# Performance work log

Hardware: AMD Instinct MI355X
Metric: run time of the kernel (lower is better)

Reference implementation:

```python
import jax, jax.numpy as jnp
import numpy as np

_J6 = jnp.array([[0,0,0,0,0,1],[0,0,0,0,-1,0],[0,0,0,1,0,0],
                 [0,0,1,0,0,0],[0,-1,0,0,0,0],[1,0,0,0,0,0]], dtype=jnp.float32)
_PAIRS4 = [(0,1),(0,2),(0,3),(1,2),(1,3),(2,3)]  # combinations(range(4),2)


def exterior(p1, p2):
    # Plucker line coords of two 4-vectors, normalized. (...,4)x(...,4)->(...,6)
    parts = [p1[..., i] * p2[..., j] - p1[..., j] * p2[..., i] for i, j in _PAIRS4]
    L = jnp.stack(parts, axis=-1)
    n = jnp.maximum(jnp.linalg.norm(L, axis=-1, keepdims=True), 1e-12)
    return L / n


def setup_inputs() -> dict:
    key = jax.random.key(0)
    B, T, D, H = 2, 2048, 1024, 16
    ks = jax.random.split(key, 10)
    w = lambda k, shape: jax.random.normal(k, shape, jnp.float32) * 0.02
    return {
        "x": jax.random.normal(ks[0], (B, T, D), jnp.float32),
        "qkv_w": w(ks[1], (3 * D, D)),
        "qkv_b": jnp.zeros((3 * D,), jnp.float32),
        "w1w": w(ks[2], (4 * H, D)),
        "w2w": w(ks[3], (4 * H, D)),
        "r1w": w(ks[4], (4 * H, D)),
        "r2w": w(ks[5], (4 * H, D)),
        "memv_w": w(ks[6], (D, D)),
        "memv_b": jnp.zeros((D,), jnp.float32),
        "memg_w": w(ks[7], (H, D)),
        "memg_b": jnp.zeros((H,), jnp.float32),
        "mem_scale": jnp.full((H,), 0.1, jnp.float32),
        "iter_mix": jnp.array(0.0, jnp.float32),
        "out_w": w(ks[8], (D, D)),
        "out_b": jnp.zeros((D,), jnp.float32),
        "decay_logits": jnp.full((H,), 4.6, jnp.float32),
    }


def reference(x, qkv_w, qkv_b, w1w, w2w, r1w, r2w, memv_w, memv_b,
              memg_w, memg_b, mem_scale, iter_mix, out_w, out_b, decay_logits):
    B, T, D = x.shape
    H = decay_logits.shape[0]
    dh = D // H
    pd = 6
    scale = dh ** -0.5

    # --- standard causal softmax attention ---
    qkv = (x @ qkv_w.T + qkv_b).reshape(B, T, 3, H, dh)
    qkv = jnp.transpose(qkv, (2, 0, 3, 1, 4))  # (3,B,H,T,dh)
    q, k, v = qkv[0], qkv[1], qkv[2]
    scores = jnp.einsum('bhtd,bhsd->bhts', q, k) * scale
    causal = jnp.triu(jnp.ones((T, T), dtype=bool), 1)
    scores = jnp.where(causal, -jnp.inf, scores)
    attn = jax.nn.softmax(scores, axis=-1)  # dropout is identity in eval
    seq_out = jnp.einsum('bhts,bhsd->bhtd', attn, v)
    seq_out = jnp.transpose(seq_out, (0, 2, 1, 3)).reshape(B, T, D)

    # --- decay-weighted Gram memory (linear-attention style state) ---
    x_prev = jnp.concatenate([jnp.zeros((B, 1, D), x.dtype), x[:, :-1]], axis=1)
    w1 = (x_prev @ w1w.T).reshape(B, T, H, 4)
    w2 = (x @ w2w.T).reshape(B, T, H, 4)
    write_lines = exterior(w1, w2)  # (B,T,H,6)
    r1 = (x @ r1w.T).reshape(B, T, H, 4)
    r2 = (x @ r2w.T).reshape(B, T, H, 4)
    read_lines = exterior(r1, r2)

    Jw = jnp.einsum('bthi,ij->bhtj', write_lines, _J6)  # (B,H,T,6)
    rd = jnp.transpose(read_lines, (0, 2, 1, 3))        # (B,H,T,6)

    decays = jax.nn.sigmoid(decay_logits)               # (H,)
    pos = jnp.arange(T, dtype=x.dtype)
    outer = Jw[..., :, None] * Jw[..., None, :]         # (B,H,T,6,6)
    decay_inv = (1.0 / jnp.maximum(decays, 1e-6))[:, None] ** pos[None, :]  # (H,T)
    outer_scaled = outer * decay_inv[None, :, :, None, None]
    M_cumsum = jnp.cumsum(outer_scaled, axis=2)
    M_cumsum = jnp.concatenate(
        [jnp.zeros((B, H, 1, pd, pd), x.dtype), M_cumsum[:, :, :-1]], axis=2)
    decay_fwd = decays[:, None] ** pos[None, :]
    M_all = M_cumsum * decay_fwd[None, :, :, None, None]

    rd_M = jnp.einsum('bhti,bhtij->bhtj', rd, M_all)
    score_M = jnp.sum(rd_M * rd, axis=-1)    # (B,H,T)
    score_M2 = jnp.sum(rd_M * rd_M, axis=-1)
    alpha = jax.nn.sigmoid(iter_mix)
    mem_score = (1 - alpha) * score_M + alpha * score_M2

    mem_val = x @ memv_w.T + memv_b                     # (B,T,D)
    gate = jax.nn.sigmoid(x @ memg_w.T + memg_b)        # (B,T,H)
    mem_score_t = jnp.transpose(mem_score, (0, 2, 1))   # (B,T,H)
    gated = jax.nn.sigmoid(mem_score_t * mem_scale) * gate
    gated = jnp.mean(gated, axis=-1, keepdims=True)     # (B,T,1)

    return (seq_out + gated * mem_val) @ out_w.T + out_b
```

## Files before the change

kernel.cpp:

```cpp
#include <hip/hip_runtime.h>
#include <stdint.h>

#define TT 2048
#define DD 1024
#define HH 16
#define LDP 4368
#define SCH 64
#define SNC (TT/SCH)

using bf16x8 = __attribute__((ext_vector_type(8))) __bf16;
using u16x8  = __attribute__((ext_vector_type(8))) unsigned short;
using f32x4  = __attribute__((ext_vector_type(4))) float;

__device__ __forceinline__ float bf2f(unsigned short u){
  unsigned int x = ((unsigned int)u) << 16;
  return __builtin_bit_cast(float, x);
}
__device__ __forceinline__ unsigned short f2bf(float f){
  unsigned int x = __builtin_bit_cast(unsigned int, f);
  x += 0x7fffu + ((x >> 16) & 1u);
  return (unsigned short)(x >> 16);
}
__device__ __forceinline__ float sigmoidf_(float x){ return 1.0f/(1.0f+__expf(-x)); }

__device__ __forceinline__ void gload_lds16(const void* g, void* l){
  auto gp = (const __attribute__((address_space(1))) unsigned int*)(uintptr_t)g;
  auto lp = (__attribute__((address_space(3))) unsigned int*)(unsigned int)(uintptr_t)l;
  __builtin_amdgcn_global_load_lds(gp, lp, 16, 0, 0);
}

__global__ void prep_all_kernel(const float* __restrict__ qkv_w, const float* __restrict__ w1w,
                                const float* __restrict__ w2w, const float* __restrict__ r1w,
                                const float* __restrict__ r2w, const float* __restrict__ memv_w,
                                const float* __restrict__ memg_w, const float* __restrict__ out_w,
                                const float* __restrict__ qkv_b, const float* __restrict__ memv_b,
                                const float* __restrict__ memg_b, const float* __restrict__ x,
                                unsigned short* __restrict__ Wcat, float* __restrict__ bcat,
                                unsigned short* __restrict__ xb)
{
  const int blk = blockIdx.x;
  if (blk < 5392) {
    const int idx = blk*256 + threadIdx.x;
    {
      const int row = idx >> 8, c4 = (idx & 255)*4;
      const float* src; int r;
      if      (row < 3072) { src = qkv_w;  r = row; }
      else if (row < 3136) { src = w1w;    r = row-3072; }
      else if (row < 3200) { src = w2w;    r = row-3136; }
      else if (row < 3264) { src = r1w;    r = row-3200; }
      else if (row < 3328) { src = r2w;    r = row-3264; }
      else if (row < 4352) { src = memv_w; r = row-3328; }
      else if (row < 4368) { src = memg_w; r = row-4352; }
      else                 { src = out_w;  r = row-4368; }
      const float4 v = *(const float4*)(src + (size_t)r*1024 + c4);
      ushort4 o; o.x=f2bf(v.x); o.y=f2bf(v.y); o.z=f2bf(v.z); o.w=f2bf(v.w);
      *(ushort4*)(Wcat + (size_t)row*1024 + c4) = o;
    }
    if (idx < 4368) {
      float v;
      if      (idx < 3072) v = qkv_b[idx];
      else if (idx < 3328) v = 0.f;
      else if (idx < 4352) v = memv_b[idx-3328];
      else                 v = memg_b[idx-4352];
      bcat[idx] = v;
    }
  } else {
    const int idx = (blk - 5392)*256 + threadIdx.x;
    const float4 v = ((const float4*)x)[idx];
    ushort4 o; o.x=f2bf(v.x); o.y=f2bf(v.y); o.z=f2bf(v.z); o.w=f2bf(v.w);
    ((ushort4*)xb)[idx] = o;
  }
}

template<bool OUTF32>
__global__ __launch_bounds__(256, 3)
void gemm_bt_kernel(const unsigned short* __restrict__ A, int lda,
                    const unsigned short* __restrict__ Bt, int ldb,
                    const float* __restrict__ bias,
                    void* __restrict__ Cout, int ldc, int N, int K)
{
  __shared__ unsigned short smem[24576];
  const int tid = threadIdx.x;
  const int w = tid >> 6, lane = tid & 63;
  const int l15 = lane & 15, l4 = lane >> 4;
  const int m0 = blockIdx.x * 128;
  const int n0 = blockIdx.y * 128;
  const int wr = (w >> 1) * 64, wc = (w & 1) * 64;

  const f32x4 zero = {0.f,0.f,0.f,0.f};
  f32x4 acc[4][4];
#pragma unroll
  for (int i = 0; i < 4; ++i)
#pragma unroll
    for (int j = 0; j < 4; ++j) acc[i][j] = zero;

  const int srow = lane >> 2;
  const int k8   = (lane & 3) * 8;

  auto stage = [&](int k0, int buf) {
#pragma unroll
    for (int q = 0; q < 4; ++q) {
      const int c = q*4 + w;
      const int rloc = (c & 7)*16 + srow;
      if (c < 8) {
        gload_lds16(A + (size_t)(m0 + rloc)*lda + k0 + k8,
                    (char*)smem + buf*8192 + (c&7)*1024);
      } else {
        int nrow = n0 + rloc; if (nrow >= N) nrow = N - 1;
        gload_lds16(Bt + (size_t)nrow*ldb + k0 + k8,
                    (char*)smem + 24576 + buf*8192 + (c&7)*1024);
      }
    }
  };

  stage(0, 0);
  if (K > 32) stage(32, 1);

  int ti = 0;
  for (int k0 = 0; k0 < K; k0 += 32, ++ti) {
    if (k0 + 32 < K) { asm volatile("s_waitcnt vmcnt(4)" ::: "memory"); }
    else             { asm volatile("s_waitcnt vmcnt(0)" ::: "memory"); }
    __builtin_amdgcn_s_barrier();
    if (k0 + 64 < K) stage(k0 + 64, (ti + 2) % 3);

    const int cur = ti % 3;
    bf16x8 af[4], bfr[4];
#pragma unroll
    for (int i = 0; i < 4; ++i) {
      af[i]  = *reinterpret_cast<const bf16x8*>((const char*)smem + cur*8192
                 + (wr + i*16 + l15)*64 + l4*16);
      bfr[i] = *reinterpret_cast<const bf16x8*>((const char*)smem + 24576 + cur*8192
                 + (wc + i*16 + l15)*64 + l4*16);
    }
#pragma unroll
    for (int i = 0; i < 4; ++i)
#pragma unroll
      for (int j = 0; j < 4; ++j)
        acc[i][j] = __builtin_amdgcn_mfma_f32_16x16x32_bf16(af[i], bfr[j], acc[i][j], 0, 0, 0);
  }

  if (OUTF32) {
#pragma unroll
    for (int i = 0; i < 4; ++i) {
      const int rowb = m0 + wr + i*16 + l4*4;
#pragma unroll
      for (int j = 0; j < 4; ++j) {
        const int col = n0 + wc + j*16 + l15;
        if (col < N) {
          const float bv = bias ? bias[col] : 0.0f;
#pragma unroll
          for (int r = 0; r < 4; ++r)
            ((float*)Cout)[(size_t)(rowb + r)*ldc + col] = acc[i][j][r] + bv;
        }
      }
    }
  } else {
    __syncthreads();
#pragma unroll
    for (int i = 0; i < 4; ++i) {
      const int rloc = wr + i*16 + l4*4;
#pragma unroll
      for (int j = 0; j < 4; ++j) {
        const int col = wc + j*16 + l15;
        const float bv = bias ? bias[n0 + col] : 0.0f;
#pragma unroll
        for (int r = 0; r < 4; ++r)
          smem[(rloc + r)*128 + col] = f2bf(acc[i][j][r] + bv);
      }
    }
    __syncthreads();
#pragma unroll
    for (int p = 0; p < 8; ++p) {
      const int idx = p*256 + tid;
      const int row = idx >> 4;
      const int c8  = (idx & 15) * 8;
      if (n0 + c8 + 8 <= N) {
        *(u16x8*)((unsigned short*)Cout + (size_t)(m0 + row)*ldc + n0 + c8) =
            *(const u16x8*)&smem[row*128 + c8];
      }
    }
  }
}

__global__ __launch_bounds__(256, 4)
void transpose_v_kernel(const unsigned short* __restrict__ P, unsigned short* __restrict__ VT)
{
  __shared__ unsigned short tile[64][66];
  const int t0 = blockIdx.x*64, h = blockIdx.y, b = blockIdx.z;
  for (int i = threadIdx.x; i < 4096; i += 256) {
    const int r = i >> 6, c = i & 63;
    tile[r][c] = P[(size_t)(b*TT + t0 + r)*LDP + 2048 + h*64 + c];
  }
  __syncthreads();
  for (int i = threadIdx.x; i < 4096; i += 256) {
    const int d = i >> 6, tl = i & 63;
    VT[(size_t)((b*HH + h)*64 + d)*TT + t0 + tl] = tile[tl][d];
  }
}

__global__ __launch_bounds__(256, 2)
void attn_kernel(const unsigned short* __restrict__ P,
                 const unsigned short* __restrict__ VT,
                 float* __restrict__ seqo)
{
  __shared__ unsigned short Ks[2][128*64];
  __shared__ unsigned short Vs[2][64*128];
  __shared__ unsigned short Pls[4][16*128];

  const int tid = threadIdx.x;
  const int w = tid >> 6, lane = tid & 63;
  const int l15 = lane & 15, l4 = lane >> 4;
  const int pi = blockIdx.x, h = blockIdx.y, b = blockIdx.z;

  auto stage = [&](int kt, int bufsel) {
#pragma unroll
    for (int q2 = 0; q2 < 4; ++q2) {
      const int idx = q2*256 + tid;
      {
        const int r = idx >> 3;
        const int cb = ((idx & 7)*16) ^ ((r & 7) << 4);
        gload_lds16(P + (size_t)(b*TT + kt*128 + r)*LDP + 1024 + h*64 + (cb >> 1),
                    (char*)Ks[bufsel] + q2*4096 + w*1024);
      }
      {
        const int r = idx >> 4;
        const int cb = ((idx & 15)*16) ^ ((r & 7) << 4);
        gload_lds16(VT + (size_t)((b*HH + h)*64 + r)*TT + kt*128 + (cb >> 1),
                    (char*)Vs[bufsel] + q2*4096 + w*1024);
      }
    }
  };

  const f32x4 zero = {0.f,0.f,0.f,0.f};
  const unsigned xorb = ((unsigned)(l15 & 7u)) << 4;

  for (int rep = 0; rep < 2; ++rep) {
    const int qt = rep == 0 ? pi : 31 - pi;
    const int qbase = qt * 64;
    const int qrow = qbase + w*16 + l15;
    const int nt = (qt >> 1) + 1;

    bf16x8 qa[2];
    {
      const size_t base = (size_t)(b*TT + qbase + w*16 + l15)*LDP + h*64 + l4*8;
      qa[0] = *reinterpret_cast<const bf16x8*>(P + base);
      qa[1] = *reinterpret_cast<const bf16x8*>(P + base + 32);
    }

    f32x4 o[4];
#pragma unroll
    for (int d = 0; d < 4; ++d) o[d] = zero;
    float mrow = -1e30f;
    float lrow = 0.f;

    stage(0, 0);
    asm volatile("s_waitcnt vmcnt(0)" ::: "memory");
    __builtin_amdgcn_s_barrier();

    for (int kt = 0; kt < nt; ++kt) {
      const int cur = kt & 1;
      if (kt + 1 < nt) stage(kt + 1, cur ^ 1);

      f32x4 s[8];
#pragma unroll
      for (int kk = 0; kk < 8; ++kk) {
        f32x4 a = zero;
#pragma unroll
        for (int c = 0; c < 2; ++c) {
          const unsigned kbyte = (unsigned)((kk*16 + l15)*128)
                               + (((unsigned)(c*64 + l4*16)) ^ xorb);
          const bf16x8 kb = *reinterpret_cast<const bf16x8*>((const char*)Ks[cur] + kbyte);
          a = __builtin_amdgcn_mfma_f32_16x16x32_bf16(kb, qa[c], a, 0, 0, 0);
        }
        s[kk] = a;
      }

      if (kt == nt - 1) {
#pragma unroll
        for (int kk = 0; kk < 8; ++kk)
#pragma unroll
          for (int j = 0; j < 4; ++j) {
            const int kcol = kt*128 + kk*16 + l4*4 + j;
            s[kk][j] = (kcol <= qrow) ? s[kk][j]*0.125f : -1e30f;
          }
      } else {
#pragma unroll
        for (int kk = 0; kk < 8; ++kk)
#pragma unroll
          for (int j = 0; j < 4; ++j) s[kk][j] *= 0.125f;
      }

      float am[8];
#pragma unroll
      for (int kk = 0; kk < 8; ++kk)
        am[kk] = fmaxf(fmaxf(s[kk][0], s[kk][1]), fmaxf(s[kk][2], s[kk][3]));
      float tmax = fmaxf(fmaxf(fmaxf(am[0], am[1]), fmaxf(am[2], am[3])),
                         fmaxf(fmaxf(am[4], am[5]), fmaxf(am[6], am[7])));
      tmax = fmaxf(tmax, __shfl_xor(tmax, 16));
      tmax = fmaxf(tmax, __shfl_xor(tmax, 32));
      const float mn = fmaxf(mrow, tmax);
      const float corr = __expf(mrow - mn);
      mrow = mn;
      float lsum = 0.f;
#pragma unroll
      for (int kk = 0; kk < 8; ++kk) {
        float p0 = __expf(s[kk][0] - mn);
        float p1 = __expf(s[kk][1] - mn);
        float p2 = __expf(s[kk][2] - mn);
        float p3 = __expf(s[kk][3] - mn);
        s[kk][0] = p0; s[kk][1] = p1; s[kk][2] = p2; s[kk][3] = p3;
        lsum += (p0 + p1) + (p2 + p3);
      }
      lsum += __shfl_xor(lsum, 16);
      lsum += __shfl_xor(lsum, 32);
      lrow = lrow*corr + lsum;

      float corrq[4];
#pragma unroll
      for (int j = 0; j < 4; ++j) corrq[j] = __shfl(corr, l4*4 + j, 16);
#pragma unroll
      for (int d = 0; d < 4; ++d)
#pragma unroll
        for (int j = 0; j < 4; ++j) o[d][j] *= corrq[j];

      const unsigned pbase = (unsigned)(w*4096);
#pragma unroll
      for (int kk = 0; kk < 8; ++kk)
#pragma unroll
        for (int jp = 0; jp < 2; ++jp) {
          const unsigned v = (unsigned)f2bf(s[kk][jp*2]) | ((unsigned)f2bf(s[kk][jp*2+1]) << 16);
          const unsigned k = (unsigned)(kk*16 + l4*4 + jp*2);
          unsigned byte = (unsigned)l15*256u + ((k*2u) ^ xorb);
          *(unsigned*)((char*)Pls + pbase + byte) = v;
        }
      asm volatile("s_waitcnt lgkmcnt(0)" ::: "memory");

#pragma unroll
      for (int c = 0; c < 4; ++c) {
        const unsigned abyte = (unsigned)(l15*256) + (((unsigned)(c*64 + l4*16)) ^ xorb);
        const bf16x8 pa = *reinterpret_cast<const bf16x8*>((char*)Pls + pbase + abyte);
#pragma unroll
        for (int d = 0; d < 4; ++d) {
          const unsigned vbyte = (unsigned)((d*16 + l15)*256)
                               + (((unsigned)(c*64 + l4*16)) ^ xorb);
          const bf16x8 vb = *reinterpret_cast<const bf16x8*>((const char*)Vs[cur] + vbyte);
          o[d] = __builtin_amdgcn_mfma_f32_16x16x32_bf16(pa, vb, o[d], 0, 0, 0);
        }
      }

      asm volatile("s_waitcnt lgkmcnt(0)" ::: "memory");
      asm volatile("s_waitcnt vmcnt(0)" ::: "memory");
      __builtin_amdgcn_s_barrier();
    }

    float lrowq[4];
#pragma unroll
    for (int j = 0; j < 4; ++j) lrowq[j] = __shfl(lrow, l4*4 + j, 16);
#pragma unroll
    for (int d = 0; d < 4; ++d)
#pragma unroll
      for (int j = 0; j < 4; ++j) {
        const int row = qbase + w*16 + l4*4 + j;
        seqo[(size_t)(b*TT + row)*DD + h*64 + d*16 + l15] = o[d][j] / lrowq[j];
      }
  }
}

__device__ __forceinline__ void ext6(const float* p, const float* q, float* L){
  L[0] = p[0]*q[1] - p[1]*q[0];
  L[1] = p[0]*q[2] - p[2]*q[0];
  L[2] = p[0]*q[3] - p[3]*q[0];
  L[3] = p[1]*q[2] - p[2]*q[1];
  L[4] = p[1]*q[3] - p[3]*q[1];
  L[5] = p[2]*q[3] - p[3]*q[2];
  const float n2 = L[0]*L[0]+L[1]*L[1]+L[2]*L[2]+L[3]*L[3]+L[4]*L[4]+L[5]*L[5];
  const float inv = 1.0f / fmaxf(sqrtf(n2), 1e-12f);
#pragma unroll
  for (int i = 0; i < 6; ++i) L[i] *= inv;
}

__global__ void exterior_kernel(const unsigned short* __restrict__ P,
                                float* __restrict__ Jw6, float* __restrict__ rd6)
{
  const int gid = blockIdx.x*256 + threadIdx.x;
  const int h = gid & 15, t = (gid >> 4) & (TT-1), b = gid >> 15;
  const size_t row = (size_t)(b*TT + t)*LDP;
  float w1[4], w2[4], r1[4], r2[4];
  if (t > 0) {
    const size_t rp = row - LDP;
#pragma unroll
    for (int j = 0; j < 4; ++j) w1[j] = bf2f(P[rp + 3072 + h*4 + j]);
  } else {
#pragma unroll
    for (int j = 0; j < 4; ++j) w1[j] = 0.f;
  }
#pragma unroll
  for (int j = 0; j < 4; ++j) {
    w2[j] = bf2f(P[row + 3136 + h*4 + j]);
    r1[j] = bf2f(P[row + 3200 + h*4 + j]);
    r2[j] = bf2f(P[row + 3264 + h*4 + j]);
  }
  float wl[6], rl[6];
  ext6(w1, w2, wl);
  ext6(r1, r2, rl);
  const float jw[6] = {wl[5], -wl[4], wl[3], wl[2], -wl[1], wl[0]};
  const size_t base = ((size_t)(b*HH + h)*TT + t)*6;
#pragma unroll
  for (int i = 0; i < 6; ++i) { Jw6[base+i] = jw[i]; rd6[base+i] = rl[i]; }
}

__global__ __launch_bounds__(64, 8)
void scan_passA(const float* __restrict__ Jw6, const float* __restrict__ decay_logits,
                float* __restrict__ E)
{
  const int bid = blockIdx.x;
  const int s = bid >> 5, c = bid & (SNC-1);
  const int lane = threadIdx.x;
  const int i = lane & 7, j = lane >> 3;
  const int ic = i < 6 ? i : 0, jc = j < 6 ? j : 0;
  const float d = sigmoidf_(decay_logits[s & (HH-1)]);
  const size_t base = ((size_t)s*TT + c*SCH)*6;
  float e = 0.f;
  for (int t = 0; t < SCH; ++t) {
    const float ai = Jw6[base + t*6 + ic];
    const float aj = Jw6[base + t*6 + jc];
    e = d*(e + ai*aj);
  }
  if (i < 6 && j < 6) E[(size_t)bid*36 + j*6 + i] = e;
}

__global__ __launch_bounds__(64, 8)
void scan_passB(const float* __restrict__ E, const float* __restrict__ decay_logits,
                float* __restrict__ BC)
{
  const int s = blockIdx.x;
  const int lane = threadIdx.x;
  if (lane >= 36) return;
  const float d = sigmoidf_(decay_logits[s & (HH-1)]);
  const float dL = __powf(d, (float)SCH);
  float bc = 0.f;
  for (int c = 0; c < SNC; ++c) {
    BC[((size_t)s*SNC + c)*36 + lane] = bc;
    bc = dL*bc + E[((size_t)s*SNC + c)*36 + lane];
  }
}

__global__ __launch_bounds__(64, 8)
void scan_passC(const float* __restrict__ Jw6, const float* __restrict__ rd6,
                const float* __restrict__ BC, const float* __restrict__ decay_logits,
                const float* __restrict__ iter_mix, float* __restrict__ msc)
{
  const int bid = blockIdx.x;
  const int s = bid >> 5, c = bid & (SNC-1);
  const int h = s & (HH-1), bb = s >> 4;
  const int lane = threadIdx.x;
  const int i = lane & 7, j = lane >> 3;
  const bool valid = (i < 6) && (j < 6);
  const int ic = i < 6 ? i : 0, jc = j < 6 ? j : 0;
  const float d = sigmoidf_(decay_logits[h]);
  const float alpha = sigmoidf_(iter_mix[0]);
  float m = 0.f;
  if (valid) m = BC[((size_t)s*SNC + c)*36 + j*6 + i];
  const size_t base = ((size_t)s*TT + c*SCH)*6;
  for (int t = 0; t < SCH; ++t) {
    const float ai = Jw6[base + t*6 + ic];
    const float aj = Jw6[base + t*6 + jc];
    const float ri = rd6[base + t*6 + ic];
    const float rj = rd6[base + t*6 + jc];
    float part = valid ? ri*m : 0.f;
    part += __shfl_xor(part, 1);
    part += __shfl_xor(part, 2);
    part += __shfl_xor(part, 4);
    float contrib = (i == 0 && j < 6) ? part*((1.f-alpha)*rj + alpha*part) : 0.f;
    contrib += __shfl_xor(contrib, 8);
    contrib += __shfl_xor(contrib, 16);
    contrib += __shfl_xor(contrib, 32);
    if (lane == 0) msc[((size_t)bb*TT + c*SCH + t)*HH + h] = contrib;
    m = d*(m + ai*aj);
  }
}

__global__ __launch_bounds__(256, 4)
void combine_kernel(const float* __restrict__ seqo, const unsigned short* __restrict__ P,
                    const float* __restrict__ msc, const float* __restrict__ mem_scale,
                    unsigned short* __restrict__ zb)
{
  const int w = threadIdx.x >> 6, lane = threadIdx.x & 63;
  const int row = blockIdx.x*4 + w;
  float val = 0.f;
  if (lane < HH) {
    const float ms = msc[(size_t)row*HH + lane];
    const float gl = bf2f(P[(size_t)row*LDP + 4352 + lane]);
    val = sigmoidf_(ms*mem_scale[lane]) * sigmoidf_(gl);
  }
  val += __shfl_xor(val, 1);
  val += __shfl_xor(val, 2);
  val += __shfl_xor(val, 4);
  val += __shfl_xor(val, 8);
  const float g = __shfl(val, 0) * (1.0f/16.0f);
#pragma unroll
  for (int it = 0; it < 4; ++it) {
    const int dcol = it*256 + lane*4;
    const float4 sv = *(const float4*)&seqo[(size_t)row*DD + dcol];
    const ushort4 pv = *(const ushort4*)&P[(size_t)row*LDP + 3328 + dcol];
    ushort4 o;
    o.x = f2bf(sv.x + g*bf2f(pv.x));
    o.y = f2bf(sv.y + g*bf2f(pv.y));
    o.z = f2bf(sv.z + g*bf2f(pv.z));
    o.w = f2bf(sv.w + g*bf2f(pv.w));
    *(ushort4*)&zb[(size_t)row*DD + dcol] = o;
  }
}

extern "C" void kernel_launch(void* const* d_in, const int* in_sizes, int n_in,
                              void* d_out, int out_size, void* d_ws, size_t ws_size,
                              hipStream_t stream)
{
  const float* x            = (const float*)d_in[0];
  const float* qkv_w        = (const float*)d_in[1];
  const float* qkv_b        = (const float*)d_in[2];
  const float* w1w          = (const float*)d_in[3];
  const float* w2w          = (const float*)d_in[4];
  const float* r1w          = (const float*)d_in[5];
  const float* r2w          = (const float*)d_in[6];
  const float* memv_w       = (const float*)d_in[7];
  const float* memv_b       = (const float*)d_in[8];
  const float* memg_w       = (const float*)d_in[9];
  const float* memg_b       = (const float*)d_in[10];
  const float* mem_scale    = (const float*)d_in[11];
  const float* iter_mix     = (const float*)d_in[12];
  const float* out_w        = (const float*)d_in[13];
  const float* out_b        = (const float*)d_in[14];
  const float* decay_logits = (const float*)d_in[15];

  char* ws = (char*)d_ws;
  unsigned short* xb   = (unsigned short*)(ws + 0);
  unsigned short* Wcat = (unsigned short*)(ws + 8388608);
  float*          bcat = (float*)         (ws + 19431424);
  unsigned short* P    = (unsigned short*)(ws + 19449088);
  unsigned short* VT   = (unsigned short*)(ws + 55231744);
  float*          seqo = (float*)         (ws + 63620352);
  float*          Jw6  = (float*)         (ws + 80397568);
  float*          rd6  = (float*)         (ws + 81970432);
  float*          E    = (float*)         (ws + 55231744);
  float*          BC   = (float*)         (ws + 55379200);
  float*          msc  = (float*)         (ws + 83690752);
  unsigned short* zb   = xb;

  prep_all_kernel<<<9488, 256, 0, stream>>>(qkv_w, w1w, w2w, r1w, r2w, memv_w, memg_w, out_w,
                                            qkv_b, memv_b, memg_b, x, Wcat, bcat, xb);
  gemm_bt_kernel<false><<<dim3(32, 35), 256, 0, stream>>>(xb, 1024, Wcat, 1024, bcat,
                                                          P, LDP, 4368, 1024);
  transpose_v_kernel<<<dim3(32, 16, 2), 256, 0, stream>>>(P, VT);
  attn_kernel<<<dim3(16, 16, 2), 256, 0, stream>>>(P, VT, seqo);
  exterior_kernel<<<256, 256, 0, stream>>>(P, Jw6, rd6);
  scan_passA<<<1024, 64, 0, stream>>>(Jw6, decay_logits, E);
  scan_passB<<<32, 64, 0, stream>>>(E, decay_logits, BC);
  scan_passC<<<1024, 64, 0, stream>>>(Jw6, rd6, BC, decay_logits, iter_mix, msc);
  combine_kernel<<<1024, 256, 0, stream>>>(seqo, P, msc, mem_scale, zb);
  gemm_bt_kernel<true><<<dim3(32, 8), 256, 0, stream>>>(zb, 1024, Wcat + (size_t)4368*1024, 1024,
                                                        out_b, d_out, 1024, 1024, 1024);
}
```

Before: 191.3 us.

## Fuse exterior computation into scan passes and fold carry scan into pass C

After: 179.8 us. 1.06x faster.

```diff
diff --git a/kernel.cpp b/kernel.cpp
--- a/kernel.cpp
+++ b/kernel.cpp
@@ -379,94 +379,92 @@
   for (int i = 0; i < 6; ++i) L[i] *= inv;
 }
 
-__global__ void exterior_kernel(const unsigned short* __restrict__ P,
-                                float* __restrict__ Jw6, float* __restrict__ rd6)
-{
-  const int gid = blockIdx.x*256 + threadIdx.x;
-  const int h = gid & 15, t = (gid >> 4) & (TT-1), b = gid >> 15;
-  const size_t row = (size_t)(b*TT + t)*LDP;
-  float w1[4], w2[4], r1[4], r2[4];
-  if (t > 0) {
-    const size_t rp = row - LDP;
-#pragma unroll
-    for (int j = 0; j < 4; ++j) w1[j] = bf2f(P[rp + 3072 + h*4 + j]);
-  } else {
-#pragma unroll
-    for (int j = 0; j < 4; ++j) w1[j] = 0.f;
-  }
-#pragma unroll
-  for (int j = 0; j < 4; ++j) {
-    w2[j] = bf2f(P[row + 3136 + h*4 + j]);
-    r1[j] = bf2f(P[row + 3200 + h*4 + j]);
-    r2[j] = bf2f(P[row + 3264 + h*4 + j]);
-  }
-  float wl[6], rl[6];
-  ext6(w1, w2, wl);
-  ext6(r1, r2, rl);
-  const float jw[6] = {wl[5], -wl[4], wl[3], wl[2], -wl[1], wl[0]};
-  const size_t base = ((size_t)(b*HH + h)*TT + t)*6;
-#pragma unroll
-  for (int i = 0; i < 6; ++i) { Jw6[base+i] = jw[i]; rd6[base+i] = rl[i]; }
+__device__ __forceinline__ void load4bf(const unsigned short* p, float* o){
+  const ushort4 u = *(const ushort4*)p;
+  o[0] = bf2f(u.x); o[1] = bf2f(u.y); o[2] = bf2f(u.z); o[3] = bf2f(u.w);
 }
 
 __global__ __launch_bounds__(64, 8)
-void scan_passA(const float* __restrict__ Jw6, const float* __restrict__ decay_logits,
+void scan_passA(const unsigned short* __restrict__ P, const float* __restrict__ decay_logits,
                 float* __restrict__ E)
 {
+  __shared__ float jwS[SCH][6];
   const int bid = blockIdx.x;
   const int s = bid >> 5, c = bid & (SNC-1);
+  const int b_ = s >> 4, h = s & (HH-1);
   const int lane = threadIdx.x;
+
+  {
+    const int t = c*SCH + lane;
+    const size_t row = (size_t)(b_*TT + t)*LDP;
+    float w1[4], w2[4];
+    if (t > 0) load4bf(P + row - LDP + 3072 + h*4, w1);
+    else { w1[0]=w1[1]=w1[2]=w1[3]=0.f; }
+    load4bf(P + row + 3136 + h*4, w2);
+    float wl[6];
+    ext6(w1, w2, wl);
+    jwS[lane][0]= wl[5]; jwS[lane][1]=-wl[4]; jwS[lane][2]= wl[3];
+    jwS[lane][3]= wl[2]; jwS[lane][4]=-wl[1]; jwS[lane][5]= wl[0];
+  }
+  __syncthreads();
+
   const int i = lane & 7, j = lane >> 3;
   const int ic = i < 6 ? i : 0, jc = j < 6 ? j : 0;
-  const float d = sigmoidf_(decay_logits[s & (HH-1)]);
-  const size_t base = ((size_t)s*TT + c*SCH)*6;
+  const float d = sigmoidf_(decay_logits[h]);
   float e = 0.f;
-  for (int t = 0; t < SCH; ++t) {
-    const float ai = Jw6[base + t*6 + ic];
-    const float aj = Jw6[base + t*6 + jc];
-    e = d*(e + ai*aj);
-  }
+  for (int t = 0; t < SCH; ++t)
+    e = d*(e + jwS[t][ic]*jwS[t][jc]);
   if (i < 6 && j < 6) E[(size_t)bid*36 + j*6 + i] = e;
 }
 
 __global__ __launch_bounds__(64, 8)
-void scan_passB(const float* __restrict__ E, const float* __restrict__ decay_logits,
-                float* __restrict__ BC)
-{
-  const int s = blockIdx.x;
-  const int lane = threadIdx.x;
-  if (lane >= 36) return;
-  const float d = sigmoidf_(decay_logits[s & (HH-1)]);
-  const float dL = __powf(d, (float)SCH);
-  float bc = 0.f;
-  for (int c = 0; c < SNC; ++c) {
-    BC[((size_t)s*SNC + c)*36 + lane] = bc;
-    bc = dL*bc + E[((size_t)s*SNC + c)*36 + lane];
-  }
-}
-
-__global__ __launch_bounds__(64, 8)
-void scan_passC(const float* __restrict__ Jw6, const float* __restrict__ rd6,
-                const float* __restrict__ BC, const float* __restrict__ decay_logits,
+void scan_passC(const unsigned short* __restrict__ P, const float* __restrict__ E,
+                const float* __restrict__ decay_logits,
                 const float* __restrict__ iter_mix, float* __restrict__ msc)
 {
+  __shared__ float Ls[SCH][12];
   const int bid = blockIdx.x;
   const int s = bid >> 5, c = bid & (SNC-1);
-  const int h = s & (HH-1), bb = s >> 4;
+  const int b_ = s >> 4, h = s & (HH-1);
   const int lane = threadIdx.x;
+
+  {
+    const int t = c*SCH + lane;
+    const size_t row = (size_t)(b_*TT + t)*LDP;
+    float w1[4], w2[4], r1[4], r2[4];
+    if (t > 0) load4bf(P + row - LDP + 3072 + h*4, w1);
+    else { w1[0]=w1[1]=w1[2]=w1[3]=0.f; }
+    load4bf(P + row + 3136 + h*4, w2);
+    load4bf(P + row + 3200 + h*4, r1);
+    load4bf(P + row + 3264 + h*4, r2);
+    float wl[6], rl[6];
+    ext6(w1, w2, wl);
+    ext6(r1, r2, rl);
+    Ls[lane][0]= wl[5]; Ls[lane][1]=-wl[4]; Ls[lane][2]= wl[3];
+    Ls[lane][3]= wl[2]; Ls[lane][4]=-wl[1]; Ls[lane][5]= wl[0];
+#pragma unroll
+    for (int q = 0; q < 6; ++q) Ls[lane][6+q] = rl[q];
+  }
+  __syncthreads();
+
   const int i = lane & 7, j = lane >> 3;
   const bool valid = (i < 6) && (j < 6);
   const int ic = i < 6 ? i : 0, jc = j < 6 ? j : 0;
   const float d = sigmoidf_(decay_logits[h]);
   const float alpha = sigmoidf_(iter_mix[0]);
+
   float m = 0.f;
-  if (valid) m = BC[((size_t)s*SNC + c)*36 + j*6 + i];
-  const size_t base = ((size_t)s*TT + c*SCH)*6;
+  if (valid) {
+    const float dL = __powf(d, (float)SCH);
+    for (int cp = 0; cp < c; ++cp)
+      m = dL*m + E[((size_t)s*SNC + cp)*36 + j*6 + i];
+  }
+
   for (int t = 0; t < SCH; ++t) {
-    const float ai = Jw6[base + t*6 + ic];
-    const float aj = Jw6[base + t*6 + jc];
-    const float ri = rd6[base + t*6 + ic];
-    const float rj = rd6[base + t*6 + jc];
+    const float ai = Ls[t][ic];
+    const float aj = Ls[t][jc];
+    const float ri = Ls[t][6+ic];
+    const float rj = Ls[t][6+jc];
     float part = valid ? ri*m : 0.f;
     part += __shfl_xor(part, 1);
     part += __shfl_xor(part, 2);
@@ -475,7 +473,7 @@
     contrib += __shfl_xor(contrib, 8);
     contrib += __shfl_xor(contrib, 16);
     contrib += __shfl_xor(contrib, 32);
-    if (lane == 0) msc[((size_t)bb*TT + c*SCH + t)*HH + h] = contrib;
+    if (lane == 0) msc[((size_t)b_*TT + c*SCH + t)*HH + h] = contrib;
     m = d*(m + ai*aj);
   }
 }
@@ -540,10 +538,7 @@
   unsigned short* P    = (unsigned short*)(ws + 19449088);
   unsigned short* VT   = (unsigned short*)(ws + 55231744);
   float*          seqo = (float*)         (ws + 63620352);
-  float*          Jw6  = (float*)         (ws + 80397568);
-  float*          rd6  = (float*)         (ws + 81970432);
-  float*          E    = (float*)         (ws + 55231744);
-  float*          BC   = (float*)         (ws + 55379200);
+  float*          E    = (float*)         (ws + 80397568);
   float*          msc  = (float*)         (ws + 83690752);
   unsigned short* zb   = xb;
 
@@ -553,10 +548,8 @@
                                                           P, LDP, 4368, 1024);
   transpose_v_kernel<<<dim3(32, 16, 2), 256, 0, stream>>>(P, VT);
   attn_kernel<<<dim3(16, 16, 2), 256, 0, stream>>>(P, VT, seqo);
-  exterior_kernel<<<256, 256, 0, stream>>>(P, Jw6, rd6);
-  scan_passA<<<1024, 64, 0, stream>>>(Jw6, decay_logits, E);
-  scan_passB<<<32, 64, 0, stream>>>(E, decay_logits, BC);
-  scan_passC<<<1024, 64, 0, stream>>>(Jw6, rd6, BC, decay_logits, iter_mix, msc);
+  scan_passA<<<1024, 64, 0, stream>>>(P, decay_logits, E);
+  scan_passC<<<1024, 64, 0, stream>>>(P, E, decay_logits, iter_mix, msc);
   combine_kernel<<<1024, 256, 0, stream>>>(seqo, P, msc, mem_scale, zb);
   gemm_bt_kernel<true><<<dim3(32, 8), 256, 0, stream>>>(zb, 1024, Wcat + (size_t)4368*1024, 1024,
                                                         out_b, d_out, 1024, 1024, 1024);
```
